# Kernel optimization log

Measured on AMD Instinct MI355X. Metric: run time of the kernel, lower is better.

Reference implementation:

```python
import jax, jax.numpy as jnp
import numpy as np

N_QUBITS = 6

def _apply_1q(state, U, w):
    # state: [B] + [2]*6 complex; U: [2,2] complex
    ax = 1 + w
    s = jnp.moveaxis(state, ax, -1)
    s = jnp.einsum('...j,ij->...i', s, U)
    return jnp.moveaxis(s, -1, ax)

def _apply_cnot(state, ctrl, tgt):
    ca, ta = 1 + ctrl, 1 + tgt
    s = jnp.moveaxis(state, (ca, ta), (1, 2))  # [B,2,2,...]
    s = jnp.stack([s[:, 0], s[:, 1, ::-1]], axis=1)
    return jnp.moveaxis(s, (1, 2), (ca, ta))

def _rot(phi, theta, omega):
    # PennyLane Rot = RZ(omega) RY(theta) RZ(phi)
    c, s = jnp.cos(theta / 2), jnp.sin(theta / 2)
    return jnp.stack([
        jnp.stack([jnp.exp(-0.5j * (phi + omega)) * c, -jnp.exp(0.5j * (phi - omega)) * s]),
        jnp.stack([jnp.exp(-0.5j * (phi - omega)) * s, jnp.exp(0.5j * (phi + omega)) * c]),
    ])

def _quantum(xq, qw):
    B = xq.shape[0]
    # AngleEmbedding RY: product state, per-qubit amplitudes [cos(x/2), sin(x/2)]
    amps = jnp.stack([jnp.cos(xq / 2), jnp.sin(xq / 2)], axis=-1)  # [B,6,2]
    state = amps[:, 0]
    for i in range(1, N_QUBITS):
        state = jnp.einsum('b...,bj->b...j', state, amps[:, i])
    state = state.astype(jnp.complex64)  # [B,2,2,2,2,2,2]
    # StronglyEntanglingLayers: per layer Rot on each wire, then CNOT ring of range r
    n_layers = qw.shape[0]
    for l in range(n_layers):
        for w in range(N_QUBITS):
            U = _rot(qw[l, w, 0], qw[l, w, 1], qw[l, w, 2])
            state = _apply_1q(state, U, w)
        r = (l % (N_QUBITS - 1)) + 1  # default ranges
        for w in range(N_QUBITS):
            state = _apply_cnot(state, w, (w + r) % N_QUBITS)
    probs = jnp.abs(state) ** 2
    zs = []
    for w in range(N_QUBITS):
        axes = tuple(a for a in range(1, N_QUBITS + 1) if a != 1 + w)
        p = jnp.sum(probs, axis=axes)  # [B,2]
        zs.append(p[:, 0] - p[:, 1])
    return jnp.stack(zs, axis=-1)  # [B,6]

def setup_inputs() -> dict:
    key = jax.random.key(0)
    ks = jax.random.split(key, 10)
    B = 16384
    return {
        'xc': jax.random.normal(ks[0], (B, 2048), jnp.float32),
        'xq': jax.random.uniform(ks[1], (B, N_QUBITS), jnp.float32),
        'W1': jax.random.normal(ks[2], (64, 2048), jnp.float32) * 0.02,
        'b1': jnp.zeros((64,), jnp.float32),
        'qw': jax.random.uniform(ks[3], (3, N_QUBITS, 3), jnp.float32, 0.0, 2 * np.pi),
        'Wq': jax.random.normal(ks[4], (16, N_QUBITS), jnp.float32) * 0.3,
        'bq': jnp.zeros((16,), jnp.float32),
        'Wf': jax.random.normal(ks[5], (3, 80), jnp.float32) * 0.1,
        'bf': jnp.zeros((3,), jnp.float32),
    }

def reference(xc, xq, W1, b1, qw, Wq, bq, Wf, bf):
    c = jax.nn.relu(xc @ W1.T + b1)                 # [B,64]
    q = _quantum(xq, qw) @ Wq.T + bq                # [B,16]
    return jnp.concatenate([c, q], axis=1) @ Wf.T + bf  # [B,3]
```

## Files before the change

### kernel.cpp

```cpp
#include <hip/hip_runtime.h>
#include <hip/hip_bf16.h>

#define NQ 6

typedef __attribute__((ext_vector_type(8))) short short8;
typedef __attribute__((ext_vector_type(4))) float floatx4;

#define WS_MQ_F   8192
#define WS_CQ_F   (8192+18)
#define WS_W1BF_B 36864

__global__ __launch_bounds__(64) void prep_kernel(
    const float* __restrict__ qw, int n_layers,
    const float* __restrict__ W1, const float* __restrict__ Wq,
    const float* __restrict__ bq, const float* __restrict__ Wf,
    const float* __restrict__ bf, float* __restrict__ ws_f,
    short* __restrict__ w1bf)
{
    const int blk  = blockIdx.x;
    const int lane = threadIdx.x;

    if (blk == 0) {
        if (lane < 18) {
            int j = lane / 6, wi = lane % 6;
            float s = 0.f;
            for (int m = 0; m < 16; ++m) s += Wf[j*80 + 64 + m] * Wq[m*6 + wi];
            ws_f[WS_MQ_F + lane] = s;
        } else if (lane < 21) {
            int j = lane - 18;
            float s = bf[j];
            for (int m = 0; m < 16; ++m) s += Wf[j*80 + 64 + m] * bq[m];
            ws_f[WS_CQ_F + j] = s;
        }
    } else if (blk <= 64) {
        const int j = blk - 1;
        float re = (lane == j) ? 1.f : 0.f;
        float im = 0.f;
        for (int l = 0; l < n_layers; ++l) {
            for (int w = 0; w < NQ; ++w) {
                const float* g = qw + (l*NQ + w)*3;
                float phi = g[0], th = g[1], om = g[2];
                float c, s;  __sincosf(0.5f*th, &s, &c);
                float sa, ca; __sincosf(0.5f*(phi+om), &sa, &ca);
                float sb, cb; __sincosf(0.5f*(phi-om), &sb, &cb);
                float u00r =  c*ca, u00i = -c*sa;
                float u01r = -s*cb, u01i = -s*sb;
                float u10r =  s*cb, u10i = -s*sb;
                float u11r =  c*ca, u11i =  c*sa;
                int p = 5 - w, mask = 1 << p;
                float pre = __shfl_xor(re, mask, 64);
                float pim = __shfl_xor(im, mask, 64);
                int b = (lane >> p) & 1;
                float mr = b ? u11r : u00r, mi = b ? u11i : u00i;
                float pr = b ? u10r : u01r, pi = b ? u10i : u01i;
                float nre = mr*re - mi*im + pr*pre - pi*pim;
                float nim = mr*im + mi*re + pr*pim + pi*pre;
                re = nre; im = nim;
            }
            int r = l % (NQ-1) + 1;
            for (int w = 0; w < NQ; ++w) {
                int tgt = (w + r) % NQ;
                int tmask = 1 << (5 - tgt);
                float pre = __shfl_xor(re, tmask, 64);
                float pim = __shfl_xor(im, tmask, 64);
                int cs = (lane >> (5 - w)) & 1;
                re = cs ? pre : re;
                im = cs ? pim : im;
            }
        }
        ws_f[(lane*64 + j)*2 + 0] = re;
        ws_f[(lane*64 + j)*2 + 1] = im;
    } else {
        int idx = (blk - 65)*512 + lane*8;
        if (idx < 64*2048) {
            float4 a0 = *(const float4*)(W1 + idx);
            float4 a1 = *(const float4*)(W1 + idx + 4);
            union { short8 v; __hip_bfloat162 h[4]; } u;
            float2 f;
            f.x=a0.x; f.y=a0.y; u.h[0] = __float22bfloat162_rn(f);
            f.x=a0.z; f.y=a0.w; u.h[1] = __float22bfloat162_rn(f);
            f.x=a1.x; f.y=a1.y; u.h[2] = __float22bfloat162_rn(f);
            f.x=a1.z; f.y=a1.w; u.h[3] = __float22bfloat162_rn(f);
            *(short8*)(w1bf + idx) = u.v;
        }
    }
}

__device__ __forceinline__ short8 cvt_bf16x8(float4 a0, float4 a1) {
    union { short8 v; __hip_bfloat162 h[4]; } u;
    float2 f;
    f.x=a0.x; f.y=a0.y; u.h[0] = __float22bfloat162_rn(f);
    f.x=a0.z; f.y=a0.w; u.h[1] = __float22bfloat162_rn(f);
    f.x=a1.x; f.y=a1.y; u.h[2] = __float22bfloat162_rn(f);
    f.x=a1.z; f.y=a1.w; u.h[3] = __float22bfloat162_rn(f);
    return u.v;
}

__global__ __launch_bounds__(512, 4) void fused_kernel(
    const float* __restrict__ xq, const float2* __restrict__ U,
    const float* __restrict__ ws_f,
    const float* __restrict__ xc, const short* __restrict__ w1bf,
    const float* __restrict__ b1, const float* __restrict__ Wf,
    float* __restrict__ out)
{
    const int tid  = threadIdx.x;
    const int lane = tid & 63;
    const int t    = __builtin_amdgcn_readfirstlane((int)(tid >> 6));
    const int blk  = blockIdx.x;

    __shared__ __align__(16) short Abuf[2][32*128];
    __shared__ float zbuf[16][32][6];
    __shared__ float qres[32][3];
    __shared__ float cl[32][65];

    const int wr = t >> 2, wc = t & 3;
    const int srow = tid >> 4;
    const int sgrp = tid & 15;
    const float* asrc = xc + (size_t)(blk*32 + srow)*2048 + sgrp*8;
    const int adoff = srow*128 + ((sgrp ^ (srow & 7)) << 3);
    const int arow = wr*16 + (lane & 15);
    const int abase = arow*128;
    const int arx = arow & 7;
    const int a_l = lane >> 4;
    const short* bp = w1bf + (wc*16 + (lane & 15))*2048 + a_l*8;

    const float* xrow = xq + (size_t)(blk*32 + (lane & 31))*6;
    float2 xq01 = *(const float2*)(xrow);
    float2 xq23 = *(const float2*)(xrow + 2);
    float2 xq45 = *(const float2*)(xrow + 4);

    float4 sA0[2], sA1[2];
    sA0[0] = *(const float4*)(asrc + 0*128);
    sA1[0] = *(const float4*)(asrc + 0*128 + 4);
    sA0[1] = *(const float4*)(asrc + 1*128);
    sA1[1] = *(const float4*)(asrc + 1*128 + 4);
    short8 bv0 = *(const short8*)(bp + 0);
    short8 bv1 = *(const short8*)(bp + 32);
    short8 bv2 = *(const short8*)(bp + 64);
    short8 bv3 = *(const short8*)(bp + 96);

    {
        const int vt = (t << 1) | (lane >> 5);
        const float xs[6] = {xq01.x, xq01.y, xq23.x, xq23.y, xq45.x, xq45.y};
        float ah[8], al[8];
        ah[0] = 1.f;
        #pragma unroll
        for (int q = 0; q < 3; ++q) {
            float c, s; __sincosf(0.5f*xs[q], &s, &c);
            const int sz = 1 << q;
            #pragma unroll
            for (int m = sz-1; m >= 0; --m) {
                float v = ah[m];
                ah[2*m+1] = v*s;
                ah[2*m+0] = v*c;
            }
        }
        al[0] = 1.f;
        #pragma unroll
        for (int q = 0; q < 3; ++q) {
            float c, s; __sincosf(0.5f*xs[3+q], &s, &c);
            const int sz = 1 << q;
            #pragma unroll
            for (int m = sz-1; m >= 0; --m) {
                float v = al[m];
                al[2*m+1] = v*s;
                al[2*m+0] = v*c;
            }
        }

        float zp[6] = {0,0,0,0,0,0};
        const float2* Urow = U + vt*4*64;
        for (int ii = 0; ii < 4; ++ii) {
            float rr = 0.f, ri = 0.f;
            #pragma unroll
            for (int jh = 0; jh < 8; ++jh) {
                float sr = 0.f, si = 0.f;
                #pragma unroll
                for (int jl = 0; jl < 8; ++jl) {
                    float2 u = Urow[ii*64 + jh*8 + jl];
                    sr += u.x * al[jl];
                    si += u.y * al[jl];
                }
                rr += ah[jh] * sr;
                ri += ah[jh] * si;
            }
            float p = rr*rr + ri*ri;
            int i = vt*4 + ii;
            #pragma unroll
            for (int w = 0; w < 6; ++w) zp[w] += ((i >> (5-w)) & 1) ? -p : p;
        }
        #pragma unroll
        for (int w = 0; w < 6; ++w) zbuf[vt][lane & 31][w] = zp[w];
    }
    __syncthreads();
    if (t == 0 && lane < 32) {
        float z[6];
        #pragma unroll
        for (int w = 0; w < 6; ++w) {
            float s = 0.f;
            #pragma unroll
            for (int sbi = 0; sbi < 16; ++sbi) s += zbuf[sbi][lane][w];
            z[w] = s;
        }
        #pragma unroll
        for (int j = 0; j < 3; ++j) {
            float v = ws_f[WS_CQ_F + j];
            #pragma unroll
            for (int w = 0; w < 6; ++w) v += ws_f[WS_MQ_F + j*6 + w] * z[w];
            qres[lane][j] = v;
        }
    }

    *(short8*)(&Abuf[0][adoff]) = cvt_bf16x8(sA0[0], sA1[0]);
    __syncthreads();

    floatx4 acc = {0,0,0,0};

    #pragma unroll
    for (int c = 0; c < 16; ++c) {
        const int cb = c & 1;

        if (c + 2 < 16) {
            sA0[cb] = *(const float4*)(asrc + (c+2)*128);
            sA1[cb] = *(const float4*)(asrc + (c+2)*128 + 4);
        }
        short8 nb0, nb1, nb2, nb3;
        if (c + 1 < 16) {
            nb0 = *(const short8*)(bp + (c+1)*128 + 0);
            nb1 = *(const short8*)(bp + (c+1)*128 + 32);
            nb2 = *(const short8*)(bp + (c+1)*128 + 64);
            nb3 = *(const short8*)(bp + (c+1)*128 + 96);
        }

        const short* abp = &Abuf[cb][abase];
        short8 av0 = *(const short8*)(abp + ((((0*4 + a_l)) ^ arx) << 3));
        short8 av1 = *(const short8*)(abp + ((((1*4 + a_l)) ^ arx) << 3));
        short8 av2 = *(const short8*)(abp + ((((2*4 + a_l)) ^ arx) << 3));
        short8 av3 = *(const short8*)(abp + ((((3*4 + a_l)) ^ arx) << 3));
        acc = __builtin_amdgcn_mfma_f32_16x16x32_bf16(av0, bv0, acc, 0, 0, 0);
        acc = __builtin_amdgcn_mfma_f32_16x16x32_bf16(av1, bv1, acc, 0, 0, 0);
        acc = __builtin_amdgcn_mfma_f32_16x16x32_bf16(av2, bv2, acc, 0, 0, 0);
        acc = __builtin_amdgcn_mfma_f32_16x16x32_bf16(av3, bv3, acc, 0, 0, 0);

        if (c + 1 < 16) {
            *(short8*)(&Abuf[cb ^ 1][adoff]) = cvt_bf16x8(sA0[cb ^ 1], sA1[cb ^ 1]);
            bv0 = nb0; bv1 = nb1; bv2 = nb2; bv3 = nb3;
            __syncthreads();
        }
    }

    const int rbase = wr*16 + (a_l * 4);
    const int c0 = wc*16 + (lane & 15);
    const float bb = b1[c0];
    #pragma unroll
    for (int r = 0; r < 4; ++r)
        cl[rbase + r][c0] = fmaxf(acc[r] + bb, 0.f);
    __syncthreads();

    const int rr2 = lane & 31;
    if (t < 3 && lane < 32) {
        float v = 0.f;
        #pragma unroll
        for (int col = 0; col < 64; ++col) v += Wf[t*80 + col] * cl[rr2][col];
        int g = blk*32 + rr2;
        out[(size_t)g*3 + t] = v + qres[rr2][t];
    }
}

extern "C" void kernel_launch(void* const* d_in, const int* in_sizes, int n_in,
                              void* d_out, int out_size, void* d_ws, size_t ws_size,
                              hipStream_t stream) {
    const float* xc = (const float*)d_in[0];
    const float* xq = (const float*)d_in[1];
    const float* W1 = (const float*)d_in[2];
    const float* b1 = (const float*)d_in[3];
    const float* qw = (const float*)d_in[4];
    const float* Wq = (const float*)d_in[5];
    const float* bq = (const float*)d_in[6];
    const float* Wf = (const float*)d_in[7];
    const float* bf = (const float*)d_in[8];
    float* out = (float*)d_out;

    const int B = in_sizes[1] / NQ;
    const int n_layers = in_sizes[4] / (NQ * 3);

    char* ws = (char*)d_ws;
    float*  ws_f  = (float*)ws;
    float2* U     = (float2*)ws;
    short*  w1bf  = (short*)(ws + WS_W1BF_B);

    prep_kernel<<<dim3(321), dim3(64), 0, stream>>>(qw, n_layers, W1, Wq, bq, Wf, bf, ws_f, w1bf);
    fused_kernel<<<dim3(B/32), dim3(512), 0, stream>>>(xq, U, ws_f, xc, w1bf, b1, Wf, out);
}
```

Measured before the change: 240.6 us.

## Stage W1 tiles in LDS via async global_load_lds and alias shared buffers

```diff
diff --git a/kernel.cpp b/kernel.cpp
--- a/kernel.cpp
+++ b/kernel.cpp
@@ -9,6 +9,9 @@
 #define WS_MQ_F   8192
 #define WS_CQ_F   (8192+18)
 #define WS_W1BF_B 36864
+
+typedef const __attribute__((address_space(1))) void gvoid_t;
+typedef __attribute__((address_space(3))) void lvoid_t;
 
 __global__ __launch_bounds__(64) void prep_kernel(
     const float* __restrict__ qw, int n_layers,
@@ -96,7 +99,7 @@
     return u.v;
 }
 
-__global__ __launch_bounds__(512, 4) void fused_kernel(
+__global__ __launch_bounds__(512, 6) void fused_kernel(
     const float* __restrict__ xq, const float2* __restrict__ U,
     const float* __restrict__ ws_f,
     const float* __restrict__ xc, const short* __restrict__ w1bf,
@@ -108,10 +111,13 @@
     const int t    = __builtin_amdgcn_readfirstlane((int)(tid >> 6));
     const int blk  = blockIdx.x;
 
-    __shared__ __align__(16) short Abuf[2][32*128];
-    __shared__ float zbuf[16][32][6];
+    __shared__ __align__(16) char  smem0[16384];
+    __shared__ __align__(16) short Bbuf[2][64*128];
     __shared__ float qres[32][3];
-    __shared__ float cl[32][65];
+
+    short* Abuf = (short*)smem0;
+    float (*zbuf)[32][6] = (float (*)[32][6])smem0;
+    float (*cl)[65]      = (float (*)[65])smem0;
 
     const int wr = t >> 2, wc = t & 3;
     const int srow = tid >> 4;
@@ -122,25 +128,28 @@
     const int abase = arow*128;
     const int arx = arow & 7;
     const int a_l = lane >> 4;
-    const short* bp = w1bf + (wc*16 + (lane & 15))*2048 + a_l*8;
+    const int bcol = wc*16 + (lane & 15);
+    const int bbase = bcol*128;
+    const int brx = bcol & 7;
+    const int dc0 = (t*2 + 0)*4 + (lane >> 4);
+    const int dc1 = (t*2 + 1)*4 + (lane >> 4);
+    const short* bsrc0 = w1bf + dc0*2048 + (((lane & 15) ^ (dc0 & 7)) << 3);
+    const short* bsrc1 = w1bf + dc1*2048 + (((lane & 15) ^ (dc1 & 7)) << 3);
 
     const float* xrow = xq + (size_t)(blk*32 + (lane & 31))*6;
     float2 xq01 = *(const float2*)(xrow);
     float2 xq23 = *(const float2*)(xrow + 2);
     float2 xq45 = *(const float2*)(xrow + 4);
 
+    __builtin_amdgcn_global_load_lds((gvoid_t*)(bsrc0 + 0*128),
+        (lvoid_t*)(&Bbuf[0][(t*2+0)*512]), 16, 0, 0);
+    __builtin_amdgcn_global_load_lds((gvoid_t*)(bsrc1 + 0*128),
+        (lvoid_t*)(&Bbuf[0][(t*2+1)*512]), 16, 0, 0);
     float4 sA0[2], sA1[2];
     sA0[0] = *(const float4*)(asrc + 0*128);
     sA1[0] = *(const float4*)(asrc + 0*128 + 4);
-    sA0[1] = *(const float4*)(asrc + 1*128);
-    sA1[1] = *(const float4*)(asrc + 1*128 + 4);
-    short8 bv0 = *(const short8*)(bp + 0);
-    short8 bv1 = *(const short8*)(bp + 32);
-    short8 bv2 = *(const short8*)(bp + 64);
-    short8 bv3 = *(const short8*)(bp + 96);
 
     {
-        const int vt = (t << 1) | (lane >> 5);
         const float xs[6] = {xq01.x, xq01.y, xq23.x, xq23.y, xq45.x, xq45.y};
         float ah[8], al[8];
         ah[0] = 1.f;
@@ -169,8 +178,8 @@
         }
 
         float zp[6] = {0,0,0,0,0,0};
-        const float2* Urow = U + vt*4*64;
-        for (int ii = 0; ii < 4; ++ii) {
+        const float2* Urow = U + t*8*64;
+        for (int ii = 0; ii < 8; ++ii) {
             float rr = 0.f, ri = 0.f;
             #pragma unroll
             for (int jh = 0; jh < 8; ++jh) {
@@ -185,12 +194,14 @@
                 ri += ah[jh] * si;
             }
             float p = rr*rr + ri*ri;
-            int i = vt*4 + ii;
+            int i = t*8 + ii;
             #pragma unroll
             for (int w = 0; w < 6; ++w) zp[w] += ((i >> (5-w)) & 1) ? -p : p;
         }
-        #pragma unroll
-        for (int w = 0; w < 6; ++w) zbuf[vt][lane & 31][w] = zp[w];
+        if (lane < 32) {
+            #pragma unroll
+            for (int w = 0; w < 6; ++w) zbuf[t][lane][w] = zp[w];
+        }
     }
     __syncthreads();
     if (t == 0 && lane < 32) {
@@ -199,7 +210,7 @@
         for (int w = 0; w < 6; ++w) {
             float s = 0.f;
             #pragma unroll
-            for (int sbi = 0; sbi < 16; ++sbi) s += zbuf[sbi][lane][w];
+            for (int sbi = 0; sbi < 8; ++sbi) s += zbuf[sbi][lane][w];
             z[w] = s;
         }
         #pragma unroll
@@ -210,8 +221,11 @@
             qres[lane][j] = v;
         }
     }
-
-    *(short8*)(&Abuf[0][adoff]) = cvt_bf16x8(sA0[0], sA1[0]);
+    sA0[1] = *(const float4*)(asrc + 1*128);
+    sA1[1] = *(const float4*)(asrc + 1*128 + 4);
+    __syncthreads();
+
+    *(short8*)(&Abuf[0*4096 + adoff]) = cvt_bf16x8(sA0[0], sA1[0]);
     __syncthreads();
 
     floatx4 acc = {0,0,0,0};
@@ -220,41 +234,44 @@
     for (int c = 0; c < 16; ++c) {
         const int cb = c & 1;
 
+        if (c + 1 < 16) {
+            __builtin_amdgcn_global_load_lds((gvoid_t*)(bsrc0 + (c+1)*128),
+                (lvoid_t*)(&Bbuf[cb ^ 1][(t*2+0)*512]), 16, 0, 0);
+            __builtin_amdgcn_global_load_lds((gvoid_t*)(bsrc1 + (c+1)*128),
+                (lvoid_t*)(&Bbuf[cb ^ 1][(t*2+1)*512]), 16, 0, 0);
+        }
         if (c + 2 < 16) {
             sA0[cb] = *(const float4*)(asrc + (c+2)*128);
             sA1[cb] = *(const float4*)(asrc + (c+2)*128 + 4);
         }
-        short8 nb0, nb1, nb2, nb3;
-        if (c + 1 < 16) {
-            nb0 = *(const short8*)(bp + (c+1)*128 + 0);
-            nb1 = *(const short8*)(bp + (c+1)*128 + 32);
-            nb2 = *(const short8*)(bp + (c+1)*128 + 64);
-            nb3 = *(const short8*)(bp + (c+1)*128 + 96);
-        }
-
-        const short* abp = &Abuf[cb][abase];
-        short8 av0 = *(const short8*)(abp + ((((0*4 + a_l)) ^ arx) << 3));
-        short8 av1 = *(const short8*)(abp + ((((1*4 + a_l)) ^ arx) << 3));
-        short8 av2 = *(const short8*)(abp + ((((2*4 + a_l)) ^ arx) << 3));
-        short8 av3 = *(const short8*)(abp + ((((3*4 + a_l)) ^ arx) << 3));
+
+        const short* abp = &Abuf[cb*4096 + abase];
+        const short* bbp = &Bbuf[cb][bbase];
+        short8 av0 = *(const short8*)(abp + (((0*4 + a_l) ^ arx) << 3));
+        short8 av1 = *(const short8*)(abp + (((1*4 + a_l) ^ arx) << 3));
+        short8 av2 = *(const short8*)(abp + (((2*4 + a_l) ^ arx) << 3));
+        short8 av3 = *(const short8*)(abp + (((3*4 + a_l) ^ arx) << 3));
+        short8 bv0 = *(const short8*)(bbp + (((0*4 + a_l) ^ brx) << 3));
+        short8 bv1 = *(const short8*)(bbp + (((1*4 + a_l) ^ brx) << 3));
+        short8 bv2 = *(const short8*)(bbp + (((2*4 + a_l) ^ brx) << 3));
+        short8 bv3 = *(const short8*)(bbp + (((3*4 + a_l) ^ brx) << 3));
         acc = __builtin_amdgcn_mfma_f32_16x16x32_bf16(av0, bv0, acc, 0, 0, 0);
         acc = __builtin_amdgcn_mfma_f32_16x16x32_bf16(av1, bv1, acc, 0, 0, 0);
         acc = __builtin_amdgcn_mfma_f32_16x16x32_bf16(av2, bv2, acc, 0, 0, 0);
         acc = __builtin_amdgcn_mfma_f32_16x16x32_bf16(av3, bv3, acc, 0, 0, 0);
 
         if (c + 1 < 16) {
-            *(short8*)(&Abuf[cb ^ 1][adoff]) = cvt_bf16x8(sA0[cb ^ 1], sA1[cb ^ 1]);
-            bv0 = nb0; bv1 = nb1; bv2 = nb2; bv3 = nb3;
+            *(short8*)(&Abuf[(cb ^ 1)*4096 + adoff]) = cvt_bf16x8(sA0[cb ^ 1], sA1[cb ^ 1]);
             __syncthreads();
         }
     }
-
-    const int rbase = wr*16 + (a_l * 4);
-    const int c0 = wc*16 + (lane & 15);
-    const float bb = b1[c0];
+    __syncthreads();
+
+    const int rbase = wr*16 + a_l*4;
+    const float bb = b1[bcol];
     #pragma unroll
     for (int r = 0; r < 4; ++r)
-        cl[rbase + r][c0] = fmaxf(acc[r] + bb, 0.f);
+        cl[rbase + r][bcol] = fmaxf(acc[r] + bb, 0.f);
     __syncthreads();
 
     const int rr2 = lane & 31;
```

Measured after the change: 220.9 us. 8.2% less time.
